# Kernel optimization log

Hardware: AMD Instinct MI355X
Metric: run time of the kernel (lower is better)

Reference implementation:

```python
import jax, jax.numpy as jnp
import numpy as np

D_MAX = 50


def setup_inputs() -> dict:
    key = jax.random.key(0)
    k1, k2, k3 = jax.random.split(key, 3)
    B, T, P, Q = 16, D_MAX + 1, 2048, 2048
    buf = jax.random.uniform(k1, (B, T, P), dtype=jnp.float32)
    weight = jax.random.normal(k2, (P, Q), dtype=jnp.float32) * np.sqrt(2.0 / P)
    delay_raw = jax.random.normal(k3, (P, Q), dtype=jnp.float32)
    return {"buf": buf, "weight": weight, "delay_raw": delay_raw}


def reference(buf, weight, delay_raw):
    # buf: [B, T, P], weight/delay_raw: [P, Q]
    d_cont = D_MAX * jax.nn.sigmoid(delay_raw)                      # [P, Q] in [0, d_max]
    d_floor = jnp.clip(jnp.floor(d_cont), 0, D_MAX).astype(jnp.int32)
    d_ceil = jnp.clip(d_floor + 1, 0, D_MAX)
    alpha = d_cont - d_floor.astype(d_cont.dtype)                   # [P, Q]

    buf_t = jnp.transpose(buf, (0, 2, 1))                           # [B, P, T]
    # per-synapse gather: s_f[b,p,q] = buf[b, d_floor[p,q], p]
    s_f = jnp.take_along_axis(buf_t, d_floor[None, :, :], axis=2)   # [B, P, Q]
    s_c = jnp.take_along_axis(buf_t, d_ceil[None, :, :], axis=2)    # [B, P, Q]
    s = (1.0 - alpha) * s_f + alpha * s_c                           # [B, P, Q]
    # weighted reduce over pre-neurons
    return jnp.einsum('bpq,pq->bq', s, weight)                      # [B, Q]
```

## Files before the change

### kernel.cpp

```cpp
#include <hip/hip_runtime.h>

#define D_MAX   50
#define T_DIM   51
#define B_DIM   16
#define P_DIM   2048
#define Q_DIM   2048
#define TSTRIDE 80
#define PBY     4112
#define PSPAN   32
#define NPBLK   (P_DIM / PSPAN)
#define QB      512


__device__ __forceinline__ float dot2bf(unsigned taps, unsigned cw, float acc) {
    float d;
    asm("v_dot2_f32_bf16 %0, %1, %2, %3" : "=v"(d) : "v"(taps), "v"(cw), "v"(acc));
    return d;
}
__device__ __forceinline__ unsigned pack_bf16x2(float lo, float hi) {
    unsigned r;
    asm("v_cvt_pk_bf16_f32 %0, %1, %2" : "=v"(r) : "v"(lo), "v"(hi));
    return r;
}

__global__ __launch_bounds__(512, 2) void dsl_fused_kernel(
    const float* __restrict__ buf, const float* __restrict__ W,
    const float* __restrict__ DR, float* __restrict__ partial) {
    __shared__ char lds[PSPAN * PBY];
    const int tid = threadIdx.x;
    const int i  = blockIdx.x;
    const int xq = i >> 6;
    const int yp = ((i & 7) << 3) | ((i >> 3) & 7);
    const int q  = xq * QB + tid;
    const int p0 = yp * PSPAN;

    const int bb = tid >> 5, pl = tid & 31;
    const float* src = buf + (size_t)bb * (T_DIM * P_DIM) + p0 + pl;
    float v[T_DIM + 1];
#pragma unroll
    for (int t = 0; t < T_DIM; ++t)
        v[t] = src[(size_t)t * P_DIM];
    v[T_DIM] = 0.f;
    {
        char* wb = lds + pl * PBY + bb * 4;
#pragma unroll
        for (int t = 0; t < T_DIM; ++t)
            *(unsigned*)(wb + t * TSTRIDE) = pack_bf16x2(v[t], v[t + 1]);
    }

    const float* Wq = W + q;
    const float* Dq = DR + q;
    float wpf[PSPAN], xpf[PSPAN];
#pragma unroll
    for (int j = 0; j < PSPAN; ++j) {
        wpf[j] = Wq[(size_t)(p0 + j) * Q_DIM];
        xpf[j] = Dq[(size_t)(p0 + j) * Q_DIM];
    }
    __syncthreads();

    float acc[B_DIM];
#pragma unroll
    for (int b = 0; b < B_DIM; ++b) acc[b] = 0.f;

#pragma unroll
    for (int p = 0; p < PSPAN; ++p) {
        const float w = wpf[p], x = xpf[p];
        const float d = 50.f / (1.f + __expf(-x));
        const int df = min((int)d, D_MAX);
        const float a  = d - (float)df;
        const float wa = w * a;
        const unsigned cw = pack_bf16x2(w - wa, wa);
        const char* rb = lds + p * PBY + df * TSTRIDE;
        const uint4 u0 = *(const uint4*)(rb);
        const uint4 u1 = *(const uint4*)(rb + 16);
        const uint4 u2 = *(const uint4*)(rb + 32);
        const uint4 u3 = *(const uint4*)(rb + 48);
        acc[0]  = dot2bf(u0.x, cw, acc[0]);
        acc[1]  = dot2bf(u0.y, cw, acc[1]);
        acc[2]  = dot2bf(u0.z, cw, acc[2]);
        acc[3]  = dot2bf(u0.w, cw, acc[3]);
        acc[4]  = dot2bf(u1.x, cw, acc[4]);
        acc[5]  = dot2bf(u1.y, cw, acc[5]);
        acc[6]  = dot2bf(u1.z, cw, acc[6]);
        acc[7]  = dot2bf(u1.w, cw, acc[7]);
        acc[8]  = dot2bf(u2.x, cw, acc[8]);
        acc[9]  = dot2bf(u2.y, cw, acc[9]);
        acc[10] = dot2bf(u2.z, cw, acc[10]);
        acc[11] = dot2bf(u2.w, cw, acc[11]);
        acc[12] = dot2bf(u3.x, cw, acc[12]);
        acc[13] = dot2bf(u3.y, cw, acc[13]);
        acc[14] = dot2bf(u3.z, cw, acc[14]);
        acc[15] = dot2bf(u3.w, cw, acc[15]);
    }

    float* dst = partial + (size_t)yp * (B_DIM * Q_DIM) + q;
#pragma unroll
    for (int b = 0; b < B_DIM; ++b)
        dst[(size_t)b * Q_DIM] = acc[b];
}

__global__ __launch_bounds__(256) void dsl_reduce_kernel(
    const float* __restrict__ partial, float* __restrict__ out) {
    __shared__ float lds[4][64];
    const int j = threadIdx.x & 63, w = threadIdx.x >> 6;
    const int idx = blockIdx.x * 64 + j;
    float s = 0.f;
    for (int c = w; c < NPBLK; c += 4)
        s += partial[(size_t)c * (B_DIM * Q_DIM) + idx];
    lds[w][j] = s;
    __syncthreads();
    if (w == 0)
        out[idx] = lds[0][j] + lds[1][j] + lds[2][j] + lds[3][j];
}

extern "C" void kernel_launch(void* const* d_in, const int* in_sizes, int n_in,
                              void* d_out, int out_size, void* d_ws, size_t ws_size,
                              hipStream_t stream) {
    const float* buf = (const float*)d_in[0];
    const float* W   = (const float*)d_in[1];
    const float* DR  = (const float*)d_in[2];
    float* out = (float*)d_out;

    float* partial = (float*)d_ws;

    hipLaunchKernelGGL(dsl_fused_kernel, dim3(256), dim3(512), 0, stream,
                       buf, W, DR, partial);
    hipLaunchKernelGGL(dsl_reduce_kernel, dim3((B_DIM * Q_DIM) / 64), dim3(256), 0, stream,
                       partial, out);
}
```

Baseline: 23.99 us.

## Halve P-span per block, reduce via atomics, drop the partial-sum reduce kernel

PSPAN is halved to 16, so the grid grows to 512 blocks (4 Q-chunks x 128 P-chunks) and occupancy rises to 4 blocks per CU. The LDS staging of buf is split over two T halves per thread to fit the smaller span. The two-pass partial-buffer reduction is replaced by a zero-fill kernel plus float atomicAdd into the output, removing the partial write and re-read. In exchange there are 128-way atomic contention per output element, nondeterministic summation order, and an extra launch.

```diff
diff --git a/kernel.cpp b/kernel.cpp
--- a/kernel.cpp
+++ b/kernel.cpp
@@ -7,10 +7,8 @@
 #define Q_DIM   2048
 #define TSTRIDE 80
 #define PBY     4112
-#define PSPAN   32
-#define NPBLK   (P_DIM / PSPAN)
+#define PSPAN   16
 #define QB      512
-
 
 __device__ __forceinline__ float dot2bf(unsigned taps, unsigned cw, float acc) {
     float d;
@@ -23,29 +21,38 @@
     return r;
 }
 
-__global__ __launch_bounds__(512, 2) void dsl_fused_kernel(
+__global__ __launch_bounds__(256) void dsl_zero_kernel(float4* __restrict__ out4) {
+    out4[blockIdx.x * 256 + threadIdx.x] = make_float4(0.f, 0.f, 0.f, 0.f);
+}
+
+__global__ __launch_bounds__(512, 4) void dsl_fused_kernel(
     const float* __restrict__ buf, const float* __restrict__ W,
-    const float* __restrict__ DR, float* __restrict__ partial) {
+    const float* __restrict__ DR, float* __restrict__ out) {
     __shared__ char lds[PSPAN * PBY];
     const int tid = threadIdx.x;
     const int i  = blockIdx.x;
-    const int xq = i >> 6;
-    const int yp = ((i & 7) << 3) | ((i >> 3) & 7);
+    const int xq = i >> 7;
+    const int yp = i & 127;
     const int q  = xq * QB + tid;
     const int p0 = yp * PSPAN;
 
-    const int bb = tid >> 5, pl = tid & 31;
-    const float* src = buf + (size_t)bb * (T_DIM * P_DIM) + p0 + pl;
-    float v[T_DIM + 1];
+    {
+        const int bb = tid >> 5, th = (tid >> 4) & 1, pl = tid & 15;
+        const int t0 = th * 26;
+        const float* src = buf + (size_t)bb * (T_DIM * P_DIM) + p0 + pl;
+        float v[27];
 #pragma unroll
-    for (int t = 0; t < T_DIM; ++t)
-        v[t] = src[(size_t)t * P_DIM];
-    v[T_DIM] = 0.f;
-    {
+        for (int j = 0; j < 27; ++j) {
+            const int t = t0 + j;
+            v[j] = (t <= 50) ? src[(size_t)t * P_DIM] : 0.f;
+        }
         char* wb = lds + pl * PBY + bb * 4;
 #pragma unroll
-        for (int t = 0; t < T_DIM; ++t)
-            *(unsigned*)(wb + t * TSTRIDE) = pack_bf16x2(v[t], v[t + 1]);
+        for (int j = 0; j < 26; ++j) {
+            const int t = t0 + j;
+            if (t <= 50)
+                *(unsigned*)(wb + t * TSTRIDE) = pack_bf16x2(v[j], v[j + 1]);
+        }
     }
 
     const float* Wq = W + q;
@@ -93,24 +100,9 @@
         acc[15] = dot2bf(u3.w, cw, acc[15]);
     }
 
-    float* dst = partial + (size_t)yp * (B_DIM * Q_DIM) + q;
 #pragma unroll
     for (int b = 0; b < B_DIM; ++b)
-        dst[(size_t)b * Q_DIM] = acc[b];
-}
-
-__global__ __launch_bounds__(256) void dsl_reduce_kernel(
-    const float* __restrict__ partial, float* __restrict__ out) {
-    __shared__ float lds[4][64];
-    const int j = threadIdx.x & 63, w = threadIdx.x >> 6;
-    const int idx = blockIdx.x * 64 + j;
-    float s = 0.f;
-    for (int c = w; c < NPBLK; c += 4)
-        s += partial[(size_t)c * (B_DIM * Q_DIM) + idx];
-    lds[w][j] = s;
-    __syncthreads();
-    if (w == 0)
-        out[idx] = lds[0][j] + lds[1][j] + lds[2][j] + lds[3][j];
+        atomicAdd(&out[(size_t)b * Q_DIM + q], acc[b]);
 }
 
 extern "C" void kernel_launch(void* const* d_in, const int* in_sizes, int n_in,
@@ -121,10 +113,8 @@
     const float* DR  = (const float*)d_in[2];
     float* out = (float*)d_out;
 
-    float* partial = (float*)d_ws;
-
-    hipLaunchKernelGGL(dsl_fused_kernel, dim3(256), dim3(512), 0, stream,
-                       buf, W, DR, partial);
-    hipLaunchKernelGGL(dsl_reduce_kernel, dim3((B_DIM * Q_DIM) / 64), dim3(256), 0, stream,
-                       partial, out);
+    hipLaunchKernelGGL(dsl_zero_kernel, dim3((B_DIM * Q_DIM / 4) / 256), dim3(256),
+                       0, stream, (float4*)out);
+    hipLaunchKernelGGL(dsl_fused_kernel, dim3(4 * 128), dim3(512), 0, stream,
+                       buf, W, DR, out);
 }
```

After: 42.84 us. +78.6%, slower.
